# Optimization experiments

Measured on AMD Instinct MI355X. Metric: run time of the kernel, lower is better.

Reference implementation:

```python
import jax, jax.numpy as jnp
import numpy as np

V = 30000   # vocab (len(en_dict))
D = 256     # embed/d_model
H = 4       # heads
DK = D // H
N = 1024    # max_len
B = 16      # batch
HID = 256   # ffn hidden
NEG = -1e10
SCALE = 1.0 / np.sqrt(DK)


def setup_inputs() -> dict:
    key = jax.random.key(0)
    ks = jax.random.split(key, 24)
    g = lambda i, shape, s=0.02: jax.random.normal(ks[i], shape, jnp.float32) * s
    return {
        'input_ids': jax.random.randint(ks[0], (B, N), 0, V),
        'attention_mask': jnp.ones((B, N), jnp.int32),
        'emb_W': g(1, (D, V)), 'emb_b': g(2, (D,)),
        'wq': g(3, (D, D)), 'bq': g(4, (D,)),
        'wk': g(5, (D, D)), 'bk': g(6, (D,)),
        'wv': g(7, (D, D)), 'bv': g(8, (D,)),
        'fc_w': g(9, (D, D)), 'fc_b': g(10, (D,)),
        'ff_w1': g(11, (HID, D)), 'ff_b1': g(12, (HID,)),
        'ff_w2': g(13, (D, HID)), 'ff_b2': g(14, (D,)),
        'h1_w': g(15, (128, D)), 'h1_b': g(16, (128,)),
        'bn_gamma': jnp.ones((128,)), 'bn_beta': jnp.zeros((128,)),
        'bn_mean': jnp.zeros((128,)), 'bn_var': jnp.ones((128,)),
        'h2_w': g(17, (1, 128)), 'h2_b': g(18, (1,)),
    }


def _pos_encoding():
    pos = jnp.arange(N, dtype=jnp.float32)[:, None]
    down = jnp.exp(jnp.arange(0, D, 2, dtype=jnp.float32) * (-np.log(10000.0) / D))
    ang = pos * down  # (N, D/2)
    pe = jnp.zeros((N, D), jnp.float32)
    pe = pe.at[:, 0::2].set(jnp.sin(ang) / 10.0)
    pe = pe.at[:, 1::2].set(jnp.cos(ang) / 10.0)
    return pe


def _forward(input_ids, attention_mask, emb_W, emb_b, wq, bq, wk, bk, wv, bv,
             fc_w, fc_b, ff_w1, ff_b1, ff_w2, ff_b2, h1_w, h1_b,
             bn_gamma, bn_beta, bn_mean, bn_var, h2_w, h2_b):
    # one-hot @ W^T + b  ==  direct column gather of W
    x = emb_W.T[input_ids] + emb_b          # (B, N, D)
    x = x + _pos_encoding()                  # dropout off (eval)

    # --- multi-head self-attention with per-sample span mask ---
    def heads(w, b):
        return (jnp.einsum('bnd,ed->bne', x, w) + b).reshape(B, N, H, DK).transpose(0, 2, 1, 3)
    q, k, v = heads(wq, bq), heads(wk, bk), heads(wv, bv)
    scores = jnp.einsum('bhnd,bhmd->bhnm', q, k) * SCALE  # (B,H,N,N)

    m = attention_mask.astype(bool)
    start = jnp.argmax(m, axis=1)                    # first True
    end = N - 1 - jnp.argmax(m[:, ::-1], axis=1)     # last True (exclusive end in slice)
    idx = jnp.arange(N)
    in_span = (idx[None, :] >= start[:, None]) & (idx[None, :] < end[:, None])  # (B,N)
    allowed = in_span[:, :, None] & in_span[:, None, :]                         # (B,N,N)
    scores = scores + jnp.where(allowed, 0.0, NEG)[:, None, :, :]

    p = jax.nn.softmax(scores, axis=-1)
    att = jnp.einsum('bhnm,bhmd->bhnd', p, v).transpose(0, 2, 1, 3).reshape(B, N, D)
    att = jnp.einsum('bnd,ed->bne', att, fc_w) + fc_b
    x = x + att

    # --- feed-forward (replaces x, no residual; dropout off; exact GELU) ---
    h = jax.nn.gelu(jnp.einsum('bnd,hd->bnh', x, ff_w1) + ff_b1, approximate=False)
    x = jnp.einsum('bnh,dh->bnd', h, ff_w2) + ff_b2

    # --- mean pool + MLP head (BatchNorm in eval mode) ---
    pooled = jnp.mean(x, axis=1)                      # (B, D)
    h = pooled @ h1_w.T + h1_b                        # (B, 128)
    h = (h - bn_mean) / jnp.sqrt(bn_var + 1e-5) * bn_gamma + bn_beta
    h = jax.nn.relu(h)
    return h @ h2_w.T + h2_b                          # (B, 1)


def reference(input_ids, attention_mask, emb_W, emb_b, wq, bq, wk, bk, wv, bv,
              fc_w, fc_b, ff_w1, ff_b1, ff_w2, ff_b2, h1_w, h1_b,
              bn_gamma, bn_beta, bn_mean, bn_var, h2_w, h2_b):
    return _forward(input_ids, attention_mask, emb_W, emb_b, wq, bq, wk, bk, wv, bv,
                    fc_w, fc_b, ff_w1, ff_b1, ff_w2, ff_b2, h1_w, h1_b,
                    bn_gamma, bn_beta, bn_mean, bn_var, h2_w, h2_b)
```

## Files before the change

kernel.cpp:

```cpp
#include <hip/hip_runtime.h>
#include <math.h>

#define VOCAB 30000
#define DMODEL 256
#define NHEAD 4
#define SEQ 1024
#define BATCH 16
#define MROWS (BATCH*SEQ)
#define SL2 0.18033688011112042f
#define NEG2 (-1.4426950408889634e10f)

typedef __attribute__((ext_vector_type(8))) short bf16x8;
typedef __attribute__((ext_vector_type(4))) float f32x4;

#if __has_builtin(__builtin_amdgcn_exp2f)
#define EXP2F __builtin_amdgcn_exp2f
#else
#define EXP2F exp2f
#endif

__device__ __forceinline__ unsigned short f2b(float f) {
    unsigned int u = __float_as_uint(f);
    unsigned int r = (u + 0x7FFFu + ((u >> 16) & 1u)) >> 16;
    return (unsigned short)r;
}
__device__ __forceinline__ unsigned short f2b_trunc(float f) {
    return (unsigned short)(__float_as_uint(f) >> 16);
}
__device__ __forceinline__ float b2f(unsigned short s) {
    unsigned int u = ((unsigned int)s) << 16;
    return __uint_as_float(u);
}

__global__ void transpose_b(const float* __restrict__ in, const float* __restrict__ eb,
                            unsigned short* __restrict__ outb) {
    __shared__ float t[32][33];
    int c0 = blockIdx.x * 32, r0 = blockIdx.y * 32;
    int tx = threadIdx.x, ty = threadIdx.y;
    for (int i = 0; i < 32; i += 8) {
        int r = r0 + ty + i, c = c0 + tx;
        if (c < VOCAB) t[ty + i][tx] = in[(size_t)r * VOCAB + c];
    }
    __syncthreads();
    float ebv = eb[r0 + tx];
    for (int i = 0; i < 32; i += 8) {
        int c = c0 + ty + i, r = r0 + tx;
        if (c < VOCAB) outb[(size_t)c * DMODEL + r] = f2b(t[tx][ty + i] + ebv);
    }
}

__global__ void prologue_kernel(const int* __restrict__ mask, int* __restrict__ spans,
                                float* __restrict__ pe,
                                const float* __restrict__ wq, const float* __restrict__ wk,
                                const float* __restrict__ wv, const float* __restrict__ bq,
                                const float* __restrict__ bk, const float* __restrict__ bv,
                                unsigned short* __restrict__ wqkv, float* __restrict__ bias768,
                                const float* __restrict__ fcw, const float* __restrict__ f1w,
                                const float* __restrict__ f2w, unsigned short* __restrict__ wb3) {
    int blk = blockIdx.x;
    int t = threadIdx.x;
    if (blk < 64) {
        __shared__ double down[128];
        if (t < 128) down[t] = exp((double)(2 * t) * (-9.210340371976184 / 256.0));
        __syncthreads();
        int d2 = t & 127, half = t >> 7;
        #pragma unroll
        for (int i = 0; i < 8; i++) {
            int n = blk * 16 + half * 8 + i;
            double ang = (double)n * down[d2];
            pe[n * DMODEL + 2 * d2]     = (float)(sin(ang) * 0.1);
            pe[n * DMODEL + 2 * d2 + 1] = (float)(cos(ang) * 0.1);
        }
    } else if (blk < 80) {
        int b = blk - 64;
        __shared__ int smin, smax;
        if (t == 0) { smin = SEQ; smax = -1; }
        __syncthreads();
        int lmin = SEQ, lmax = -1;
        for (int i = t; i < SEQ; i += 256) {
            if (mask[b * SEQ + i] != 0) { lmin = min(lmin, i); lmax = max(lmax, i); }
        }
        atomicMin(&smin, lmin);
        atomicMax(&smax, lmax);
        __syncthreads();
        if (t == 0) {
            int st, en;
            if (smax < 0) { st = 0; en = SEQ - 1; }
            else          { st = smin; en = smax; }
            spans[b * 2] = st; spans[b * 2 + 1] = en;
        }
    } else if (blk < 849) {
        int cb = blk - 80;
        if (cb < 768) {
            const float* src = (cb < 256) ? wq : (cb < 512) ? wk : wv;
            wqkv[cb * 256 + t] = f2b(src[(cb & 255) * 256 + t]);
        } else {
            for (int j = t; j < 768; j += 256)
                bias768[j] = (j < 256) ? bq[j] : (j < 512) ? bk[j - 256] : bv[j - 512];
        }
    } else {
        int cb = blk - 849;
        const float* src = (cb < 256) ? fcw : (cb < 512) ? f1w : f2w;
        wb3[cb * 256 + t] = f2b(src[(cb & 255) * 256 + t]);
    }
}

__global__ void embed_kernel(const int* __restrict__ ids, const unsigned short* __restrict__ embT,
                             const float* __restrict__ pe, unsigned short* __restrict__ x0b) {
    int bn = blockIdx.x;
    int d = threadIdx.x;
    int id = ids[bn];
    int n = bn & (SEQ - 1);
    float v = b2f(embT[(size_t)id * DMODEL + d]) + pe[n * DMODEL + d];
    x0b[(size_t)bn * DMODEL + d] = f2b(v);
}

__global__ __launch_bounds__(512) void qkv_kernel(const unsigned short* __restrict__ A,
                                                  const unsigned short* __restrict__ W,
                                                  const float* __restrict__ bias,
                                                  unsigned short* __restrict__ Qb,
                                                  unsigned short* __restrict__ Kb,
                                                  unsigned short* __restrict__ Vt) {
    __shared__ unsigned short XA[4 * 64 * 64];
    __shared__ unsigned short Bs[2][256 * 64];
    int tid = threadIdx.x;
    int m0 = blockIdx.x * 64;
    int w = tid >> 6, l = tid & 63;
    int wrow = w >> 1, wcol = w & 1;
    int lg = l >> 4, ll = l & 15;
    int bb = m0 >> 10;

    #pragma unroll
    for (int i = 0; i < 4; i++) {
        int s = tid + i * 512;
        int row = s >> 5;
        int kb = (s & 31) * 16;
        int kt = kb >> 7, within = kb & 127;
        int swz = within ^ ((row & 7) << 4);
        float4 av = *(const float4*)((const char*)A + (size_t)(m0 + row) * 512 + kb);
        *(float4*)((char*)XA + kt * 8192 + row * 128 + swz) = av;
    }

    for (int nb = 0; nb < 3; nb++) {
        f32x4 acc[8] = {};
        #pragma unroll
        for (int i = 0; i < 4; i++) {
            int s = tid + i * 512;
            int row = s >> 3, kb = (s & 7) * 16;
            int swz = kb ^ ((row & 7) << 4);
            float4 bv = *(const float4*)((const char*)W + (size_t)(nb * 256 + row) * 512 + kb);
            *(float4*)((char*)Bs[0] + row * 128 + swz) = bv;
        }
        __syncthreads();

        for (int kt = 0; kt < 4; kt++) {
            int cur = kt & 1;
            float4 pre[4];
            if (kt < 3) {
                #pragma unroll
                for (int i = 0; i < 4; i++) {
                    int s = tid + i * 512;
                    int row = s >> 3, kb = (s & 7) * 16;
                    pre[i] = *(const float4*)((const char*)W + (size_t)(nb * 256 + row) * 512 + (kt + 1) * 128 + kb);
                }
            }
            int arow = wrow * 16 + ll;
            bf16x8 af[2];
            #pragma unroll
            for (int ks = 0; ks < 2; ks++)
                af[ks] = *(const bf16x8*)((const char*)XA + kt * 8192 + arow * 128 + ((lg * 16 + ks * 64) ^ ((arow & 7) << 4)));
            #pragma unroll
            for (int nf = 0; nf < 8; nf++) {
                int brow = wcol * 128 + nf * 16 + ll;
                #pragma unroll
                for (int ks = 0; ks < 2; ks++) {
                    bf16x8 bf = *(const bf16x8*)((const char*)Bs[cur] + brow * 128 + ((lg * 16 + ks * 64) ^ ((brow & 7) << 4)));
                    acc[nf] = __builtin_amdgcn_mfma_f32_16x16x32_bf16(af[ks], bf, acc[nf], 0, 0, 0);
                }
            }
            if (kt < 3) {
                #pragma unroll
                for (int i = 0; i < 4; i++) {
                    int s = tid + i * 512;
                    int row = s >> 3, kb = (s & 7) * 16;
                    int swz = kb ^ ((row & 7) << 4);
                    *(float4*)((char*)Bs[cur ^ 1] + row * 128 + swz) = pre[i];
                }
            }
            __syncthreads();
        }
        #pragma unroll
        for (int nf = 0; nf < 8; nf++) {
            int col = wcol * 128 + nf * 16 + ll;
            float bv = bias[nb * 256 + col];
            int hh = col >> 6, dk = col & 63;
            if (nb == 2) {
                unsigned int lo = (unsigned int)f2b(acc[nf][0] + bv) | ((unsigned int)f2b(acc[nf][1] + bv) << 16);
                unsigned int hi = (unsigned int)f2b(acc[nf][2] + bv) | ((unsigned int)f2b(acc[nf][3] + bv) << 16);
                int ns = (m0 & 1023) + wrow * 16 + lg * 4;
                unsigned int* dst = (unsigned int*)(Vt + ((((size_t)bb * 4 + hh) * 64) + dk) * 1024 + ns);
                dst[0] = lo;
                dst[1] = hi;
            } else {
                #pragma unroll
                for (int r2 = 0; r2 < 4; r2++) {
                    int ns = (m0 & 1023) + wrow * 16 + lg * 4 + r2;
                    float v = acc[nf][r2] + bv;
                    if (nb == 0)
                        Qb[((((size_t)bb * 4 + hh) * 1024) + ns) * 64 + dk] = f2b(v * SL2);
                    else
                        Kb[((((size_t)bb * 4 + hh) * 1024) + ns) * 64 + dk] = f2b(v);
                }
            }
        }
    }
}

__global__ __launch_bounds__(512) void attn_coop(const unsigned short* __restrict__ Qb,
                                                 const unsigned short* __restrict__ Kb,
                                                 const unsigned short* __restrict__ Vt,
                                                 const int* __restrict__ spans,
                                                 unsigned short* __restrict__ attb) {
    __shared__ unsigned short Ks[64 * 64];
    __shared__ unsigned short Vs[64 * 64];
    __shared__ __align__(16) unsigned short Ps[8][16 * 72];
    int tid = threadIdx.x;
    int w = tid >> 6, l = tid & 63;
    int id = blockIdx.x;
    int c = id & 7, rest = id >> 3;
    int bh = c * 8 + (rest >> 3);
    int qg = rest & 7;
    int q0 = qg * 128 + w * 16;
    int b = bh >> 2, h = bh & 3;
    int lg = l >> 4, ll = l & 15;
    const char* Kp = (const char*)(Kb + (size_t)bh * SEQ * 64);
    const char* Vp = (const char*)(Vt + (size_t)bh * 64 * SEQ);
    const unsigned short* Qp = Qb + (size_t)bh * SEQ * 64;
    int start = spans[b * 2], end = spans[b * 2 + 1];

    bf16x8 qf[2];
    #pragma unroll
    for (int ks = 0; ks < 2; ks++)
        qf[ks] = *(const bf16x8*)(Qp + (size_t)(q0 + ll) * 64 + lg * 8 + ks * 32);

    bf16x8 ones;
    #pragma unroll
    for (int i = 0; i < 8; i++) ones[i] = (short)0x3F80;

    f32x4 o[4] = {};
    f32x4 accl = {};
    bool rowok[4];
    #pragma unroll
    for (int r2 = 0; r2 < 4; r2++) {
        int rr = q0 + lg * 4 + r2;
        rowok[r2] = (rr >= start) && (rr < end);
    }

    for (int ct = 0; ct < 16; ct++) {
        int kv0 = ct * 64;

        {
            int s = tid;
            int row = s >> 3;
            int kb = (s & 7) * 16;
            int swz = kb ^ ((row & 7) << 4);
            float4 kvv = *(const float4*)(Kp + (size_t)(kv0 + row) * 128 + kb);
            *(float4*)((char*)Ks + row * 128 + swz) = kvv;
            float4 vvv = *(const float4*)(Vp + (size_t)row * 2048 + kv0 * 2 + kb);
            *(float4*)((char*)Vs + row * 128 + swz) = vvv;
        }
        __syncthreads();

        f32x4 s4[4];
        #pragma unroll
        for (int nf = 0; nf < 4; nf++) {
            int cc = kv0 + nf * 16 + ll;
            float ci = ((cc >= start) && (cc < end)) ? 0.f : NEG2;
            f32x4 cv = { ci, ci, ci, ci };
            s4[nf] = cv;
        }
        #pragma unroll
        for (int ks = 0; ks < 2; ks++)
            #pragma unroll
            for (int nf = 0; nf < 4; nf++) {
                int row = nf * 16 + ll;
                bf16x8 kf = *(const bf16x8*)((const char*)Ks + row * 128 + ((lg * 16 + ks * 64) ^ ((row & 7) << 4)));
                s4[nf] = __builtin_amdgcn_mfma_f32_16x16x32_bf16(qf[ks], kf, s4[nf], 0, 0, 0);
            }

        #pragma unroll
        for (int nf = 0; nf < 4; nf++)
            #pragma unroll
            for (int r2 = 0; r2 < 4; r2++) {
                float sv = rowok[r2] ? s4[nf][r2] : 0.f;
                s4[nf][r2] = EXP2F(sv);
            }

        #pragma unroll
        for (int nf = 0; nf < 4; nf++)
            #pragma unroll
            for (int r2 = 0; r2 < 4; r2++)
                Ps[w][(lg * 4 + r2) * 72 + nf * 16 + ll] = f2b_trunc(s4[nf][r2]);

        bf16x8 pa[2];
        #pragma unroll
        for (int ks = 0; ks < 2; ks++)
            pa[ks] = *(const bf16x8*)(&Ps[w][ll * 72 + lg * 8 + ks * 32]);

        #pragma unroll
        for (int ks = 0; ks < 2; ks++)
            #pragma unroll
            for (int cf = 0; cf < 4; cf++) {
                int row = cf * 16 + ll;
                bf16x8 vf = *(const bf16x8*)((const char*)Vs + row * 128 + ((lg * 16 + ks * 64) ^ ((row & 7) << 4)));
                o[cf] = __builtin_amdgcn_mfma_f32_16x16x32_bf16(pa[ks], vf, o[cf], 0, 0, 0);
            }
        #pragma unroll
        for (int ks = 0; ks < 2; ks++)
            accl = __builtin_amdgcn_mfma_f32_16x16x32_bf16(pa[ks], ones, accl, 0, 0, 0);

        __syncthreads();
    }

    #pragma unroll
    for (int r2 = 0; r2 < 4; r2++) {
        float inv = 1.f / accl[r2];
        int row = q0 + lg * 4 + r2;
        #pragma unroll
        for (int cf = 0; cf < 4; cf++) {
            int dk = cf * 16 + ll;
            attb[((size_t)b * SEQ + row) * 256 + h * 64 + dk] = f2b(o[cf][r2] * inv);
        }
    }
}

__global__ __launch_bounds__(512) void ffn_kernel(const unsigned short* __restrict__ attb,
                                                  const unsigned short* __restrict__ x0b,
                                                  const unsigned short* __restrict__ W3,
                                                  const float* __restrict__ fcb,
                                                  const float* __restrict__ f1b,
                                                  const float* __restrict__ f2bv,
                                                  float* __restrict__ part) {
    __shared__ unsigned short BufA[4 * 64 * 64];
    __shared__ unsigned short BufB[4 * 64 * 64];
    __shared__ unsigned short Bs[2][256 * 64];
    int tid = threadIdx.x;
    int m0 = blockIdx.x * 64;
    int w = tid >> 6, l = tid & 63;
    int wrow = w >> 1, wcol = w & 1;
    int lg = l >> 4, ll = l & 15;
    int arow = wrow * 16 + ll;

    #pragma unroll
    for (int i = 0; i < 4; i++) {
        int s = tid + i * 512;
        int row = s >> 5;
        int kb = (s & 31) * 16;
        int kt = kb >> 7, within = kb & 127;
        int swz = within ^ ((row & 7) << 4);
        float4 av = *(const float4*)((const char*)attb + (size_t)(m0 + row) * 512 + kb);
        *(float4*)((char*)BufA + kt * 8192 + row * 128 + swz) = av;
    }

    #pragma unroll
    for (int phase = 0; phase < 3; phase++) {
        const unsigned short* Wp = W3 + phase * 65536;
        const char* Asrc = (phase == 1) ? (const char*)BufB : (const char*)BufA;
        f32x4 acc[8] = {};
        #pragma unroll
        for (int i = 0; i < 4; i++) {
            int s = tid + i * 512;
            int row = s >> 3, kb = (s & 7) * 16;
            int swz = kb ^ ((row & 7) << 4);
            float4 bv = *(const float4*)((const char*)Wp + (size_t)row * 512 + kb);
            *(float4*)((char*)Bs[0] + row * 128 + swz) = bv;
        }
        __syncthreads();

        for (int kt = 0; kt < 4; kt++) {
            int cur = kt & 1;
            float4 pre[4];
            if (kt < 3) {
                #pragma unroll
                for (int i = 0; i < 4; i++) {
                    int s = tid + i * 512;
                    int row = s >> 3, kb = (s & 7) * 16;
                    pre[i] = *(const float4*)((const char*)Wp + (size_t)row * 512 + (kt + 1) * 128 + kb);
                }
            }
            bf16x8 af[2];
            #pragma unroll
            for (int ks = 0; ks < 2; ks++)
                af[ks] = *(const bf16x8*)(Asrc + kt * 8192 + arow * 128 + ((lg * 16 + ks * 64) ^ ((arow & 7) << 4)));
            #pragma unroll
            for (int nf = 0; nf < 8; nf++) {
                int brow = wcol * 128 + nf * 16 + ll;
                #pragma unroll
                for (int ks = 0; ks < 2; ks++) {
                    bf16x8 bf = *(const bf16x8*)((const char*)Bs[cur] + brow * 128 + ((lg * 16 + ks * 64) ^ ((brow & 7) << 4)));
                    acc[nf] = __builtin_amdgcn_mfma_f32_16x16x32_bf16(af[ks], bf, acc[nf], 0, 0, 0);
                }
            }
            if (kt < 3) {
                #pragma unroll
                for (int i = 0; i < 4; i++) {
                    int s = tid + i * 512;
                    int row = s >> 3, kb = (s & 7) * 16;
                    int swz = kb ^ ((row & 7) << 4);
                    *(float4*)((char*)Bs[cur ^ 1] + row * 128 + swz) = pre[i];
                }
            }
            __syncthreads();
        }

        if (phase == 0) {
            #pragma unroll
            for (int nf = 0; nf < 8; nf++) {
                int col = wcol * 128 + nf * 16 + ll;
                float bv = fcb[col];
                int kt = col >> 6;
                int byteoff = (2 * (col & 63));
                #pragma unroll
                for (int r2 = 0; r2 < 4; r2++) {
                    int row = wrow * 16 + lg * 4 + r2;
                    *(unsigned short*)((char*)BufB + kt * 8192 + row * 128 + (byteoff ^ ((row & 7) << 4))) = f2b(acc[nf][r2] + bv);
                }
            }
            __syncthreads();
            #pragma unroll
            for (int i = 0; i < 4; i++) {
                int s = tid + i * 512;
                int row = s >> 5;
                int kb = (s & 31) * 16;
                int kt = kb >> 7, within = kb & 127;
                int swz = within ^ ((row & 7) << 4);
                bf16x8* dst = (bf16x8*)((char*)BufB + kt * 8192 + row * 128 + swz);
                bf16x8 xv = *dst;
                bf16x8 rv = *(const bf16x8*)((const char*)x0b + (size_t)(m0 + row) * 512 + kb);
                bf16x8 res;
                #pragma unroll
                for (int jj = 0; jj < 8; jj++)
                    res[jj] = (short)f2b(b2f((unsigned short)xv[jj]) + b2f((unsigned short)rv[jj]));
                *dst = res;
            }
        } else if (phase == 1) {
            #pragma unroll
            for (int nf = 0; nf < 8; nf++) {
                int col = wcol * 128 + nf * 16 + ll;
                float bv = f1b[col];
                int kt = col >> 6;
                int byteoff = (2 * (col & 63));
                #pragma unroll
                for (int r2 = 0; r2 < 4; r2++) {
                    int row = wrow * 16 + lg * 4 + r2;
                    float v = acc[nf][r2] + bv;
                    v = 0.5f * v * (1.f + erff(v * 0.70710678118654752f));
                    *(unsigned short*)((char*)BufA + kt * 8192 + row * 128 + (byteoff ^ ((row & 7) << 4))) = f2b(v);
                }
            }
        } else {
            int bb = m0 >> 10;
            int chunk = ((m0 & 1023) >> 4) + wrow;
            #pragma unroll
            for (int nf = 0; nf < 8; nf++) {
                int col = wcol * 128 + nf * 16 + ll;
                float s_ = acc[nf][0] + acc[nf][1] + acc[nf][2] + acc[nf][3];
                s_ += __shfl_xor(s_, 16);
                s_ += __shfl_xor(s_, 32);
                s_ += 16.f * f2bv[col];
                if (lg == 0)
                    part[((size_t)bb * 64 + chunk) * 256 + col] = s_;
            }
        }
    }
}

__global__ __launch_bounds__(128) void head2_kernel(const float* __restrict__ part,
                                                    const float* __restrict__ h1_w, const float* __restrict__ h1_b,
                                                    const float* __restrict__ g, const float* __restrict__ be,
                                                    const float* __restrict__ mu, const float* __restrict__ var,
                                                    const float* __restrict__ h2_w, const float* __restrict__ h2_b,
                                                    float* __restrict__ out) {
    int b = blockIdx.x, j = threadIdx.x;
    __shared__ float pl[256];
    __shared__ float red[128];
    float s0 = 0.f, s1 = 0.f;
    for (int ch = 0; ch < 64; ch++) {
        s0 += part[((size_t)b * 64 + ch) * 256 + j];
        s1 += part[((size_t)b * 64 + ch) * 256 + j + 128];
    }
    pl[j] = s0 * (1.f / 1024.f);
    pl[j + 128] = s1 * (1.f / 1024.f);
    __syncthreads();
    float s = 0.f;
    for (int d = 0; d < 256; d++) s = fmaf(pl[d], h1_w[j * 256 + d], s);
    s += h1_b[j];
    s = (s - mu[j]) / sqrtf(var[j] + 1e-5f) * g[j] + be[j];
    s = fmaxf(s, 0.f);
    red[j] = s * h2_w[j];
    __syncthreads();
    for (int off = 64; off; off >>= 1) {
        if (j < off) red[j] += red[j + off];
        __syncthreads();
    }
    if (j == 0) out[b] = red[0] + h2_b[0];
}

extern "C" void kernel_launch(void* const* d_in, const int* in_sizes, int n_in,
                              void* d_out, int out_size, void* d_ws, size_t ws_size,
                              hipStream_t stream) {
    (void)in_sizes; (void)n_in; (void)out_size; (void)ws_size;
    const int*   ids    = (const int*)d_in[0];
    const int*   amask  = (const int*)d_in[1];
    const float* emb_W  = (const float*)d_in[2];
    const float* emb_b  = (const float*)d_in[3];
    const float* wq = (const float*)d_in[4],  *bq = (const float*)d_in[5];
    const float* wk = (const float*)d_in[6],  *bk = (const float*)d_in[7];
    const float* wv = (const float*)d_in[8],  *bv = (const float*)d_in[9];
    const float* fcw = (const float*)d_in[10], *fcb = (const float*)d_in[11];
    const float* f1w = (const float*)d_in[12], *f1b = (const float*)d_in[13];
    const float* f2w = (const float*)d_in[14], *f2b_ = (const float*)d_in[15];
    const float* h1w = (const float*)d_in[16], *h1b = (const float*)d_in[17];
    const float* bng = (const float*)d_in[18], *bnb = (const float*)d_in[19];
    const float* bnm = (const float*)d_in[20], *bnv = (const float*)d_in[21];
    const float* h2w = (const float*)d_in[22], *h2b = (const float*)d_in[23];
    float* out = (float*)d_out;
    float* ws = (float*)d_ws;

    const size_t O_PE   = 0;
    const size_t O_EMBT = O_PE + 262144;
    const size_t O_X0B  = O_EMBT + 3840000;
    const size_t O_Q    = O_X0B + 2097152;
    const size_t O_K    = O_Q + 2097152;
    const size_t O_V    = O_K + 2097152;
    const size_t O_ATT  = O_V + 2097152;
    const size_t O_WQKV = O_ATT + 2097152;
    const size_t O_WB3  = O_WQKV + 98304;
    const size_t O_B768 = O_WB3 + 98304;
    const size_t O_PART = O_B768 + 768;
    const size_t O_SPAN = O_PART + 262144;

    float* pe   = ws + O_PE;
    unsigned short* embT = (unsigned short*)(ws + O_EMBT);
    unsigned short* x0b  = (unsigned short*)(ws + O_X0B);
    unsigned short* Qb   = (unsigned short*)(ws + O_Q);
    unsigned short* Kb   = (unsigned short*)(ws + O_K);
    unsigned short* Vt   = (unsigned short*)(ws + O_V);
    unsigned short* attb = (unsigned short*)(ws + O_ATT);
    unsigned short* wqkv = (unsigned short*)(ws + O_WQKV);
    unsigned short* wb3  = (unsigned short*)(ws + O_WB3);
    float* bias768 = ws + O_B768;
    float* part = ws + O_PART;
    int* spans  = (int*)(ws + O_SPAN);

    dim3 tb(32, 8);
    prologue_kernel<<<1617, 256, 0, stream>>>(amask, spans, pe,
                                              wq, wk, wv, bq, bk, bv, wqkv, bias768,
                                              fcw, f1w, f2w, wb3);
    transpose_b<<<dim3((VOCAB + 31) / 32, 8), tb, 0, stream>>>(emb_W, emb_b, embT);
    embed_kernel<<<MROWS, 256, 0, stream>>>(ids, embT, pe, x0b);

    qkv_kernel<<<256, 512, 0, stream>>>(x0b, wqkv, bias768, Qb, Kb, Vt);

    attn_coop<<<512, 512, 0, stream>>>(Qb, Kb, Vt, spans, attb);

    ffn_kernel<<<256, 512, 0, stream>>>(attb, x0b, wb3, fcb, f1b, f2b_, part);

    head2_kernel<<<BATCH, 128, 0, stream>>>(part, h1w, h1b, bng, bnb, bnm, bnv, h2w, h2b, out);
}
```

Before: 110.1 us.

## Double-buffer K/V tiles in attention and merge transpose into prologue kernel

The attention kernel now keeps two shared-memory K/V buffers and issues the global loads for the next tile into registers before the current tile's MFMA work. It writes them to the other buffer afterwards, so only one barrier is needed per iteration and load latency overlaps with compute. Separately, the embedding transpose is folded into the prologue kernel as extra blocks, removing one launch and letting the two run concurrently. The cost is double the K/V shared memory and more live registers in attention.

Result: faster. 100.1 us (-9.0%).

```diff
diff --git a/kernel.cpp b/kernel.cpp
--- a/kernel.cpp
+++ b/kernel.cpp
@@ -32,31 +32,16 @@
     return __uint_as_float(u);
 }
 
-__global__ void transpose_b(const float* __restrict__ in, const float* __restrict__ eb,
-                            unsigned short* __restrict__ outb) {
-    __shared__ float t[32][33];
-    int c0 = blockIdx.x * 32, r0 = blockIdx.y * 32;
-    int tx = threadIdx.x, ty = threadIdx.y;
-    for (int i = 0; i < 32; i += 8) {
-        int r = r0 + ty + i, c = c0 + tx;
-        if (c < VOCAB) t[ty + i][tx] = in[(size_t)r * VOCAB + c];
-    }
-    __syncthreads();
-    float ebv = eb[r0 + tx];
-    for (int i = 0; i < 32; i += 8) {
-        int c = c0 + ty + i, r = r0 + tx;
-        if (c < VOCAB) outb[(size_t)c * DMODEL + r] = f2b(t[tx][ty + i] + ebv);
-    }
-}
-
-__global__ void prologue_kernel(const int* __restrict__ mask, int* __restrict__ spans,
-                                float* __restrict__ pe,
-                                const float* __restrict__ wq, const float* __restrict__ wk,
-                                const float* __restrict__ wv, const float* __restrict__ bq,
-                                const float* __restrict__ bk, const float* __restrict__ bv,
-                                unsigned short* __restrict__ wqkv, float* __restrict__ bias768,
-                                const float* __restrict__ fcw, const float* __restrict__ f1w,
-                                const float* __restrict__ f2w, unsigned short* __restrict__ wb3) {
+__global__ __launch_bounds__(256) void prep_kernel(const int* __restrict__ mask, int* __restrict__ spans,
+                                                   float* __restrict__ pe,
+                                                   const float* __restrict__ wq, const float* __restrict__ wk,
+                                                   const float* __restrict__ wv, const float* __restrict__ bq,
+                                                   const float* __restrict__ bk, const float* __restrict__ bv,
+                                                   unsigned short* __restrict__ wqkv, float* __restrict__ bias768,
+                                                   const float* __restrict__ fcw, const float* __restrict__ f1w,
+                                                   const float* __restrict__ f2w, unsigned short* __restrict__ wb3,
+                                                   const float* __restrict__ embW, const float* __restrict__ eb,
+                                                   unsigned short* __restrict__ embT) {
     int blk = blockIdx.x;
     int t = threadIdx.x;
     if (blk < 64) {
@@ -98,10 +83,26 @@
             for (int j = t; j < 768; j += 256)
                 bias768[j] = (j < 256) ? bq[j] : (j < 512) ? bk[j - 256] : bv[j - 512];
         }
-    } else {
+    } else if (blk < 1617) {
         int cb = blk - 849;
         const float* src = (cb < 256) ? fcw : (cb < 512) ? f1w : f2w;
         wb3[cb * 256 + t] = f2b(src[(cb & 255) * 256 + t]);
+    } else {
+        __shared__ float tsh[32][33];
+        int tb = blk - 1617;
+        int bx = tb % 938, by = tb / 938;
+        int tx = t & 31, ty = t >> 5;
+        int c0 = bx * 32, r0 = by * 32;
+        for (int i = 0; i < 32; i += 8) {
+            int r = r0 + ty + i, c = c0 + tx;
+            if (c < VOCAB) tsh[ty + i][tx] = embW[(size_t)r * VOCAB + c];
+        }
+        __syncthreads();
+        float ebv = eb[r0 + tx];
+        for (int i = 0; i < 32; i += 8) {
+            int c = c0 + ty + i, r = r0 + tx;
+            if (c < VOCAB) embT[(size_t)c * DMODEL + r] = f2b(tsh[tx][ty + i] + ebv);
+        }
     }
 }
 
@@ -221,8 +222,8 @@
                                                  const unsigned short* __restrict__ Vt,
                                                  const int* __restrict__ spans,
                                                  unsigned short* __restrict__ attb) {
-    __shared__ unsigned short Ks[64 * 64];
-    __shared__ unsigned short Vs[64 * 64];
+    __shared__ unsigned short Ks[2][64 * 64];
+    __shared__ unsigned short Vs[2][64 * 64];
     __shared__ __align__(16) unsigned short Ps[8][16 * 72];
     int tid = threadIdx.x;
     int w = tid >> 6, l = tid & 63;
@@ -256,20 +257,27 @@
         rowok[r2] = (rr >= start) && (rr < end);
     }
 
+    int srow = tid >> 3, skb = (tid & 7) * 16;
+    int sswz = skb ^ ((srow & 7) << 4);
+
+    {
+        float4 kv0v = *(const float4*)(Kp + (size_t)srow * 128 + skb);
+        float4 vv0 = *(const float4*)(Vp + (size_t)srow * 2048 + skb);
+        *(float4*)((char*)Ks[0] + srow * 128 + sswz) = kv0v;
+        *(float4*)((char*)Vs[0] + srow * 128 + sswz) = vv0;
+    }
+
     for (int ct = 0; ct < 16; ct++) {
+        int cur = ct & 1;
         int kv0 = ct * 64;
-
-        {
-            int s = tid;
-            int row = s >> 3;
-            int kb = (s & 7) * 16;
-            int swz = kb ^ ((row & 7) << 4);
-            float4 kvv = *(const float4*)(Kp + (size_t)(kv0 + row) * 128 + kb);
-            *(float4*)((char*)Ks + row * 128 + swz) = kvv;
-            float4 vvv = *(const float4*)(Vp + (size_t)row * 2048 + kv0 * 2 + kb);
-            *(float4*)((char*)Vs + row * 128 + swz) = vvv;
-        }
-        __syncthreads();
+        __syncthreads();
+
+        float4 kreg, vreg;
+        if (ct < 15) {
+            int kvn = kv0 + 64;
+            kreg = *(const float4*)(Kp + (size_t)(kvn + srow) * 128 + skb);
+            vreg = *(const float4*)(Vp + (size_t)srow * 2048 + kvn * 2 + skb);
+        }
 
         f32x4 s4[4];
         #pragma unroll
@@ -284,7 +292,7 @@
             #pragma unroll
             for (int nf = 0; nf < 4; nf++) {
                 int row = nf * 16 + ll;
-                bf16x8 kf = *(const bf16x8*)((const char*)Ks + row * 128 + ((lg * 16 + ks * 64) ^ ((row & 7) << 4)));
+                bf16x8 kf = *(const bf16x8*)((const char*)Ks[cur] + row * 128 + ((lg * 16 + ks * 64) ^ ((row & 7) << 4)));
                 s4[nf] = __builtin_amdgcn_mfma_f32_16x16x32_bf16(qf[ks], kf, s4[nf], 0, 0, 0);
             }
 
@@ -312,14 +320,17 @@
             #pragma unroll
             for (int cf = 0; cf < 4; cf++) {
                 int row = cf * 16 + ll;
-                bf16x8 vf = *(const bf16x8*)((const char*)Vs + row * 128 + ((lg * 16 + ks * 64) ^ ((row & 7) << 4)));
+                bf16x8 vf = *(const bf16x8*)((const char*)Vs[cur] + row * 128 + ((lg * 16 + ks * 64) ^ ((row & 7) << 4)));
                 o[cf] = __builtin_amdgcn_mfma_f32_16x16x32_bf16(pa[ks], vf, o[cf], 0, 0, 0);
             }
         #pragma unroll
         for (int ks = 0; ks < 2; ks++)
             accl = __builtin_amdgcn_mfma_f32_16x16x32_bf16(pa[ks], ones, accl, 0, 0, 0);
 
-        __syncthreads();
+        if (ct < 15) {
+            *(float4*)((char*)Ks[cur ^ 1] + srow * 128 + sswz) = kreg;
+            *(float4*)((char*)Vs[cur ^ 1] + srow * 128 + sswz) = vreg;
+        }
     }
 
     #pragma unroll
@@ -553,11 +564,10 @@
     float* part = ws + O_PART;
     int* spans  = (int*)(ws + O_SPAN);
 
-    dim3 tb(32, 8);
-    prologue_kernel<<<1617, 256, 0, stream>>>(amask, spans, pe,
-                                              wq, wk, wv, bq, bk, bv, wqkv, bias768,
-                                              fcw, f1w, f2w, wb3);
-    transpose_b<<<dim3((VOCAB + 31) / 32, 8), tb, 0, stream>>>(emb_W, emb_b, embT);
+    prep_kernel<<<1617 + 938 * 8, 256, 0, stream>>>(amask, spans, pe,
+                                                    wq, wk, wv, bq, bk, bv, wqkv, bias768,
+                                                    fcw, f1w, f2w, wb3,
+                                                    emb_W, emb_b, embT);
     embed_kernel<<<MROWS, 256, 0, stream>>>(ids, embT, pe, x0b);
 
     qkv_kernel<<<256, 512, 0, stream>>>(x0b, wqkv, bias768, Qb, Kb, Vt);
```
